# Kernel optimization log

Measured on AMD Instinct MI355X. Metric: run time of the kernel, lower is better.

## Reference

```python
import jax, jax.numpy as jnp
import numpy as np

EPS = 1e-5


def _lstm_agg(x, nbr_idx, Wih, Whh, bih, bhh):
    # x: [N, D] node feats; nbr_idx: [N, K]; LSTM hidden size == D (DGL lstm aggregator)
    seq = x[nbr_idx]                     # [N, K, D] irregular gather
    N, K, D = seq.shape
    seq_t = jnp.swapaxes(seq, 0, 1)      # [K, N, D] time-major for scan

    def step(carry, xt):
        h, c = carry
        z = xt @ Wih.T + bih + h @ Whh.T + bhh   # [N, 4D]; torch gate order i,f,g,o
        i, f, g, o = jnp.split(z, 4, axis=-1)
        i = jax.nn.sigmoid(i)
        f = jax.nn.sigmoid(f)
        g = jnp.tanh(g)
        o = jax.nn.sigmoid(o)
        c = f * c + i * g
        h = o * jnp.tanh(c)
        return (h, c), None

    zero = jnp.zeros((N, D), seq.dtype)
    (h, _), _ = jax.lax.scan(step, (zero, zero), seq_t)
    return h                             # final hidden state = neighbor aggregate


def _sage_layer(x, nbr_idx, Wih, Whh, bih, bhh, Wself, bself, Wneigh):
    h_neigh = _lstm_agg(x, nbr_idx, Wih, Whh, bih, bhh)
    return x @ Wself.T + bself + h_neigh @ Wneigh.T


def _bn(x, gamma, beta):
    # BatchNorm1d in training mode: batch statistics over the node axis
    mu = jnp.mean(x, axis=0)
    var = jnp.var(x, axis=0)
    return (x - mu) * jax.lax.rsqrt(var + EPS) * gamma + beta


def setup_inputs() -> dict:
    key = jax.random.key(0)
    N, K, D_IN, D_H = 100000, 16, 128, 128
    ks = jax.random.split(key, 20)
    s = 0.05
    inp = {
        "in_feat": jax.random.normal(ks[0], (N, D_IN), jnp.float32),
        "nbr_idx": jax.random.randint(ks[1], (N, K), 0, N, jnp.int32),
        # layer 1 (in_feats=128 -> h_feats=128), LSTM hidden = in_feats
        "Wih1": jax.random.normal(ks[2], (4 * D_IN, D_IN), jnp.float32) * s,
        "Whh1": jax.random.normal(ks[3], (4 * D_IN, D_IN), jnp.float32) * s,
        "bih1": jnp.zeros((4 * D_IN,), jnp.float32),
        "bhh1": jnp.zeros((4 * D_IN,), jnp.float32),
        "Wself1": jax.random.normal(ks[4], (D_H, D_IN), jnp.float32) * s,
        "bself1": jnp.zeros((D_H,), jnp.float32),
        "Wneigh1": jax.random.normal(ks[5], (D_H, D_IN), jnp.float32) * s,
        "gamma1": jnp.ones((D_H,), jnp.float32),
        "beta1": jnp.zeros((D_H,), jnp.float32),
        # layer 2 (h_feats=128 -> h_feats=128)
        "Wih2": jax.random.normal(ks[6], (4 * D_H, D_H), jnp.float32) * s,
        "Whh2": jax.random.normal(ks[7], (4 * D_H, D_H), jnp.float32) * s,
        "bih2": jnp.zeros((4 * D_H,), jnp.float32),
        "bhh2": jnp.zeros((4 * D_H,), jnp.float32),
        "Wself2": jax.random.normal(ks[8], (D_H, D_H), jnp.float32) * s,
        "bself2": jnp.zeros((D_H,), jnp.float32),
        "Wneigh2": jax.random.normal(ks[9], (D_H, D_H), jnp.float32) * s,
        "gamma2": jnp.ones((D_H,), jnp.float32),
        "beta2": jnp.zeros((D_H,), jnp.float32),
    }
    return inp


def reference(in_feat, nbr_idx,
              Wih1, Whh1, bih1, bhh1, Wself1, bself1, Wneigh1, gamma1, beta1,
              Wih2, Whh2, bih2, bhh2, Wself2, bself2, Wneigh2, gamma2, beta2):
    h = _sage_layer(in_feat, nbr_idx, Wih1, Whh1, bih1, bhh1, Wself1, bself1, Wneigh1)
    h = jax.nn.relu(_bn(h, gamma1, beta1))
    h = _sage_layer(h, nbr_idx, Wih2, Whh2, bih2, bhh2, Wself2, bself2, Wneigh2)
    h = _bn(h, gamma2, beta2)
    return h
```

## Files before the change

kernel.cpp:

```cpp
#include <hip/hip_runtime.h>

typedef unsigned short u16;
typedef unsigned int u32;
typedef unsigned long long u64;
typedef __attribute__((ext_vector_type(8))) short short8;
typedef __attribute__((ext_vector_type(4))) float float4_t;

__device__ __forceinline__ float bf2f(u16 v) {
    union { u32 u; float f; } x; x.u = ((u32)v) << 16; return x.f;
}
__device__ __forceinline__ u16 f2bf(float f) {
    union { float f; u32 u; } x; x.f = f;
    u32 r = x.u + 0x7FFFu + ((x.u >> 16) & 1u);
    return (u16)(r >> 16);
}
__device__ __forceinline__ u32 pk2bf(float hi, float lo) {
    union { float f; u32 u; } a, b; a.f = hi; b.f = lo;
    return __builtin_amdgcn_perm(a.u + 0x8000u, b.u + 0x8000u, 0x07060302u);
}
#define LOG2E 1.44269504088896340736f
__device__ __forceinline__ float sigm(float x) {
    return __builtin_amdgcn_rcpf(1.f + __builtin_amdgcn_exp2f(-LOG2E * x));
}
__device__ __forceinline__ float tanh_(float x) {
    float t = __builtin_amdgcn_exp2f(2.f * LOG2E * x);
    return 1.f - 2.f * __builtin_amdgcn_rcpf(1.f + t);
}

__device__ __forceinline__ float4_t mfma16(short8 a, short8 b, float4_t c) {
    return __builtin_amdgcn_mfma_f32_16x16x32_bf16(a, b, c, 0, 0, 0);
}

__device__ __forceinline__ short8 ldfrag(const u16* p) { return *(const short8*)p; }
__device__ __forceinline__ short8 ldfrag(const float* p) {
    float4_t a = *(const float4_t*)p;
    float4_t b = *(const float4_t*)(p + 4);
    short8 r;
#pragma unroll
    for (int j = 0; j < 4; ++j) { r[j] = (short)f2bf(a[j]); r[4 + j] = (short)f2bf(b[j]); }
    return r;
}

template<typename AT>
__global__ __launch_bounds__(256) void gemm_ih(
    const AT* __restrict__ A, const float* __restrict__ W,
    const float* __restrict__ b1, const float* __restrict__ b2,
    u16* __restrict__ C, int M)
{
    const int P = 512;
    const int lane = threadIdx.x & 63;
    const int w    = threadIdx.x >> 6;
    const int l15  = lane & 15;
    const int quad = lane >> 4;
    const int rowbase = blockIdx.x * 64;
    const int colbase = blockIdx.y * 128 + w * 32;

    short8 af[4][4];
#pragma unroll
    for (int mb = 0; mb < 4; ++mb) {
        int row = rowbase + mb * 16 + l15;
        if (row >= M) row = M - 1;
        const AT* ap = A + (size_t)row * 128 + quad * 8;
#pragma unroll
        for (int kb = 0; kb < 4; ++kb) af[mb][kb] = ldfrag(ap + kb * 32);
    }
    short8 bfr[2][4];
#pragma unroll
    for (int nb = 0; nb < 2; ++nb) {
        int col = colbase + nb * 16 + l15;
        const float* wp = W + (size_t)col * 128 + quad * 8;
#pragma unroll
        for (int kb = 0; kb < 4; ++kb) bfr[nb][kb] = ldfrag(wp + kb * 32);
    }
    const float4_t z4 = {0.f, 0.f, 0.f, 0.f};
    float bias[2];
#pragma unroll
    for (int nb = 0; nb < 2; ++nb) {
        int col = colbase + nb * 16 + l15;
        bias[nb] = b1[col] + b2[col];
    }
#pragma unroll
    for (int mb = 0; mb < 4; ++mb)
#pragma unroll
        for (int nb = 0; nb < 2; ++nb) {
            float4_t a = z4;
#pragma unroll
            for (int kb = 0; kb < 4; ++kb) a = mfma16(af[mb][kb], bfr[nb][kb], a);
#pragma unroll
            for (int r = 0; r < 4; ++r) {
                int row = rowbase + mb * 16 + quad * 4 + r;
                int col = colbase + nb * 16 + l15;
                if (row < M) C[(size_t)row * P + col] = f2bf(a[r] + bias[nb]);
            }
        }
}

template<typename T>
__device__ __forceinline__ void accum_gemm(
    const T* __restrict__ A, const float* __restrict__ W,
    float4_t (&acc)[4][2], int M, int rowbase, int colbase, int l15, int quad)
{
    short8 af[4][4];
#pragma unroll
    for (int mb = 0; mb < 4; ++mb) {
        int row = rowbase + mb * 16 + l15;
        if (row >= M) row = M - 1;
        const T* ap = A + (size_t)row * 128 + quad * 8;
#pragma unroll
        for (int kb = 0; kb < 4; ++kb) af[mb][kb] = ldfrag(ap + kb * 32);
    }
    short8 bfr[2][4];
#pragma unroll
    for (int nb = 0; nb < 2; ++nb) {
        int col = colbase + nb * 16 + l15;
        const float* wp = W + (size_t)col * 128 + quad * 8;
#pragma unroll
        for (int kb = 0; kb < 4; ++kb) bfr[nb][kb] = ldfrag(wp + kb * 32);
    }
#pragma unroll
    for (int mb = 0; mb < 4; ++mb)
#pragma unroll
        for (int nb = 0; nb < 2; ++nb)
#pragma unroll
            for (int kb = 0; kb < 4; ++kb)
                acc[mb][nb] = mfma16(af[mb][kb], bfr[nb][kb], acc[mb][nb]);
}

template<typename AT2>
__global__ __launch_bounds__(256) void gemm_out(
    const u16* __restrict__ A1, const float* __restrict__ W1,
    const AT2* __restrict__ A2, const float* __restrict__ W2,
    const float* __restrict__ bias, float* __restrict__ C,
    float* __restrict__ stats, int M)
{
    const int P = 128;
    const int lane = threadIdx.x & 63;
    const int w    = threadIdx.x >> 6;
    const int l15  = lane & 15;
    const int quad = lane >> 4;
    const int rowbase = blockIdx.x * 64;
    const int colbase = w * 32;

    float4_t acc[4][2];
    const float4_t z4 = {0.f, 0.f, 0.f, 0.f};
#pragma unroll
    for (int mb = 0; mb < 4; ++mb)
#pragma unroll
        for (int nb = 0; nb < 2; ++nb) acc[mb][nb] = z4;

    accum_gemm(A1, W1, acc, M, rowbase, colbase, l15, quad);
    accum_gemm(A2, W2, acc, M, rowbase, colbase, l15, quad);

    float s[2] = {0.f, 0.f}, sq[2] = {0.f, 0.f};
#pragma unroll
    for (int nb = 0; nb < 2; ++nb) {
        int col = colbase + nb * 16 + l15;
        float bb = bias[col];
#pragma unroll
        for (int mb = 0; mb < 4; ++mb)
#pragma unroll
            for (int r = 0; r < 4; ++r) {
                int row = rowbase + mb * 16 + quad * 4 + r;
                if (row < M) {
                    float v = acc[mb][nb][r] + bb;
                    C[(size_t)row * P + col] = v;
                    s[nb] += v; sq[nb] += v * v;
                }
            }
    }
#pragma unroll
    for (int nb = 0; nb < 2; ++nb) {
        float t1 = s[nb], t2 = sq[nb];
        t1 += __shfl_xor(t1, 16); t1 += __shfl_xor(t1, 32);
        t2 += __shfl_xor(t2, 16); t2 += __shfl_xor(t2, 32);
        int col = colbase + nb * 16 + l15;
        if (quad == 0) atomicAdd(&stats[col], t1);
        if (quad == 1) atomicAdd(&stats[P + col], t2);
    }
}

__global__ __launch_bounds__(512, 2) void lstm_kernel(
    const u16* __restrict__ Xih,
    const int* __restrict__ nbr,
    const float* __restrict__ Whh,
    u16* __restrict__ Hout,
    int N)
{
    __shared__ u16 hbuf[2][64][136];
    __shared__ int nbrs[16][72];
    const int tid  = threadIdx.x;
    const int lane = tid & 63;
    const int w    = tid >> 6;
    const int l15  = lane & 15;
    const int quad = lane >> 4;
    const int base = blockIdx.x * 64;

    short8 whA[4][4];
#pragma unroll
    for (int g = 0; g < 4; ++g) {
        int row = 128 * g + 16 * w + l15;
        const float* wp = Whh + (size_t)row * 128 + quad * 8;
#pragma unroll
        for (int kb = 0; kb < 4; ++kb) whA[g][kb] = ldfrag(wp + kb * 32);
    }
    short8 I;
    {
        int off = (w & 1) ? 16 : 0;
#pragma unroll
        for (int j = 0; j < 8; ++j) {
            int k = quad * 8 + j;
            I[j] = (short)((k == l15 + off) ? 0x3F80 : 0);
        }
    }
    u32* hz = (u32*)&hbuf[0][0][0];
    for (int i = tid; i < 2 * 64 * 136 / 2; i += 512) hz[i] = 0u;
    for (int i = tid; i < 64 * 16; i += 512) {
        int node = base + (i >> 4);
        if (node >= N) node = N - 1;
        nbrs[i & 15][i >> 4] = nbr[(size_t)node * 16 + (i & 15)];
    }
    __syncthreads();

    const int xcol0 = 32 * (w >> 1);
    short8 xf[4][4];
#pragma unroll
    for (int nb = 0; nb < 4; ++nb) {
        int node = nbrs[0][l15 + 16 * nb];
        const u16* xp = Xih + (size_t)node * 512 + xcol0 + quad * 8;
#pragma unroll
        for (int g = 0; g < 4; ++g) xf[nb][g] = *(const short8*)(xp + 128 * g);
    }

    const float4_t z4 = {0.f, 0.f, 0.f, 0.f};
    float4_t c[4];
#pragma unroll
    for (int nb = 0; nb < 4; ++nb) c[nb] = z4;
    float4_t hlast[4];

    for (int t = 0; t < 16; ++t) {
        const int p = t & 1;
#pragma unroll
        for (int nb = 0; nb < 4; ++nb) {
            const u16* hp = &hbuf[p][l15 + 16 * nb][quad * 8];
            short8 hb[4];
#pragma unroll
            for (int kb = 0; kb < 4; ++kb) hb[kb] = *(const short8*)(hp + kb * 32);
            float4_t z[4];
#pragma unroll
            for (int g = 0; g < 4; ++g) z[g] = mfma16(I, xf[nb][g], z4);
            if (t < 15) {
                int node = nbrs[t + 1][l15 + 16 * nb];
                const u16* xp = Xih + (size_t)node * 512 + xcol0 + quad * 8;
#pragma unroll
                for (int g = 0; g < 4; ++g) xf[nb][g] = *(const short8*)(xp + 128 * g);
            }
#pragma unroll
            for (int g = 0; g < 4; ++g)
#pragma unroll
                for (int kb = 0; kb < 4; ++kb)
                    z[g] = mfma16(whA[g][kb], hb[kb], z[g]);
            float4_t hv;
#pragma unroll
            for (int r = 0; r < 4; ++r) {
                float i_ = sigm(z[0][r]);
                float f_ = sigm(z[1][r]);
                float g_ = tanh_(z[2][r]);
                float o_ = sigm(z[3][r]);
                float cc = f_ * c[nb][r] + i_ * g_;
                c[nb][r] = cc;
                hv[r] = o_ * tanh_(cc);
            }
            hlast[nb] = hv;
            u64 pkd = ((u64)pk2bf(hv[3], hv[2]) << 32) | pk2bf(hv[1], hv[0]);
            *(u64*)&hbuf[1 - p][l15 + 16 * nb][16 * w + quad * 4] = pkd;
        }
        __syncthreads();
    }
#pragma unroll
    for (int nb = 0; nb < 4; ++nb) {
        int row = base + l15 + 16 * nb;
        if (row < N) {
            u64 pkd = ((u64)pk2bf(hlast[nb][3], hlast[nb][2]) << 32)
                      | pk2bf(hlast[nb][1], hlast[nb][0]);
            *(u64*)(Hout + (size_t)row * 128 + 16 * w + quad * 4) = pkd;
        }
    }
}

__global__ void zero_stats(float* s) { s[threadIdx.x] = 0.f; }

__global__ void bn_prep(float* stats, const float* __restrict__ gamma,
                        const float* __restrict__ beta, float invN)
{
    int cidx = threadIdx.x;
    float s = stats[cidx], sq = stats[128 + cidx];
    float mu = s * invN;
    float var = sq * invN - mu * mu;
    float sc = gamma[cidx] * rsqrtf(var + 1e-5f);
    stats[256 + cidx] = sc;
    stats[384 + cidx] = beta[cidx] - mu * sc;
}

template<typename OT>
__global__ __launch_bounds__(256) void bn_apply(
    const float* __restrict__ X, const float* __restrict__ stats,
    OT* __restrict__ Y, int M, int relu)
{
    int gid = blockIdx.x * 256 + threadIdx.x;
    int row = gid >> 4;
    int cs  = (gid & 15) * 8;
    if (row >= M) return;
    float4_t a = *(const float4_t*)(X + (size_t)row * 128 + cs);
    float4_t b = *(const float4_t*)(X + (size_t)row * 128 + cs + 4);
    float v[8];
#pragma unroll
    for (int j = 0; j < 8; ++j) {
        float x = (j < 4) ? a[j] : b[j - 4];
        float t = x * stats[256 + cs + j] + stats[384 + cs + j];
        v[j] = relu ? fmaxf(t, 0.f) : t;
    }
    if constexpr (sizeof(OT) == 2) {
        short8 ov;
#pragma unroll
        for (int j = 0; j < 8; ++j) ov[j] = (short)f2bf(v[j]);
        *(short8*)((u16*)Y + (size_t)row * 128 + cs) = ov;
    } else {
        float4_t o1, o2;
#pragma unroll
        for (int j = 0; j < 4; ++j) { o1[j] = v[j]; o2[j] = v[4 + j]; }
        *(float4_t*)((float*)Y + (size_t)row * 128 + cs) = o1;
        *(float4_t*)((float*)Y + (size_t)row * 128 + cs + 4) = o2;
    }
}

extern "C" void kernel_launch(void* const* d_in, const int* in_sizes, int n_in,
                              void* d_out, int out_size, void* d_ws, size_t ws_size,
                              hipStream_t stream)
{
    const float* in_feat = (const float*)d_in[0];
    const int*   nbr     = (const int*)d_in[1];
    const float* Wih1 = (const float*)d_in[2];
    const float* Whh1 = (const float*)d_in[3];
    const float* bih1 = (const float*)d_in[4];
    const float* bhh1 = (const float*)d_in[5];
    const float* Wself1  = (const float*)d_in[6];
    const float* bself1  = (const float*)d_in[7];
    const float* Wneigh1 = (const float*)d_in[8];
    const float* gamma1  = (const float*)d_in[9];
    const float* beta1   = (const float*)d_in[10];
    const float* Wih2 = (const float*)d_in[11];
    const float* Whh2 = (const float*)d_in[12];
    const float* bih2 = (const float*)d_in[13];
    const float* bhh2 = (const float*)d_in[14];
    const float* Wself2  = (const float*)d_in[15];
    const float* bself2  = (const float*)d_in[16];
    const float* Wneigh2 = (const float*)d_in[17];
    const float* gamma2  = (const float*)d_in[18];
    const float* beta2   = (const float*)d_in[19];

    const int N = in_sizes[0] / 128;

    char* ws = (char*)d_ws;
    u16*   Xih   = (u16*)ws;
    float* Pbuf  = (float*)ws;
    u16*   hn    = (u16*)(ws + (size_t)N * 1024);
    float* stats = (float*)(ws + (size_t)N * 1024 + (size_t)N * 256);
    u16*   hcur  = (u16*)d_out;

    const int nblk = (N + 63) / 64;
    const float invN = 1.0f / (float)N;
    const int bnblk = (N * 16 + 255) / 256;

    zero_stats<<<dim3(1), dim3(256), 0, stream>>>(stats);
    gemm_ih<float><<<dim3(nblk, 4), dim3(256), 0, stream>>>(in_feat, Wih1, bih1, bhh1, Xih, N);
    lstm_kernel<<<dim3(nblk), dim3(512), 0, stream>>>(Xih, nbr, Whh1, hn, N);
    gemm_out<float><<<dim3(nblk, 1), dim3(256), 0, stream>>>(hn, Wneigh1, in_feat, Wself1,
                                                             bself1, Pbuf, stats, N);
    bn_prep<<<dim3(1), dim3(128), 0, stream>>>(stats, gamma1, beta1, invN);
    bn_apply<u16><<<dim3(bnblk), dim3(256), 0, stream>>>(Pbuf, stats, hcur, N, 1);

    zero_stats<<<dim3(1), dim3(256), 0, stream>>>(stats);
    gemm_ih<u16><<<dim3(nblk, 4), dim3(256), 0, stream>>>(hcur, Wih2, bih2, bhh2, Xih, N);
    lstm_kernel<<<dim3(nblk), dim3(512), 0, stream>>>(Xih, nbr, Whh2, hn, N);
    gemm_out<u16><<<dim3(nblk, 1), dim3(256), 0, stream>>>(hn, Wneigh2, hcur, Wself2,
                                                           bself2, Pbuf, stats, N);
    bn_prep<<<dim3(1), dim3(128), 0, stream>>>(stats, gamma2, beta2, invN);
    bn_apply<float><<<dim3(bnblk), dim3(256), 0, stream>>>(Pbuf, stats, (float*)d_out, N, 0);
}
```

Before: 1.683 ms.

## Permute Xih columns to match MFMA output layout and add input term directly

The input-projection GEMM now writes its output columns in a permuted order, so each LSTM lane can load its own gate pre-activations with two contiguous 16-byte loads. These values are unpacked from bf16 and added in fp32, which removes the identity-matrix MFMA that was used only to inject the input projection into the accumulator. The change also raises launch bounds to 4 blocks per SM, pads the hidden-state LDS rows to reduce bank conflicts, and moves the barrier to the start of each timestep. Higher occupancy may cause register spills, and correctness now depends on the column permutation matching the lane mapping exactly.

```diff
diff --git a/kernel.cpp b/kernel.cpp
--- a/kernel.cpp
+++ b/kernel.cpp
@@ -5,6 +5,7 @@
 typedef unsigned long long u64;
 typedef __attribute__((ext_vector_type(8))) short short8;
 typedef __attribute__((ext_vector_type(4))) float float4_t;
+typedef __attribute__((ext_vector_type(4))) u32 uint4_t;
 
 __device__ __forceinline__ float bf2f(u16 v) {
     union { u32 u; float f; } x; x.u = ((u32)v) << 16; return x.f;
@@ -39,6 +40,11 @@
 #pragma unroll
     for (int j = 0; j < 4; ++j) { r[j] = (short)f2bf(a[j]); r[4 + j] = (short)f2bf(b[j]); }
     return r;
+}
+
+__device__ __forceinline__ int origcol(int n) {
+    int g = (n >> 2) & 3, w = n >> 6, q = (n >> 4) & 3, r = n & 3;
+    return 128 * g + 16 * w + 4 * q + r;
 }
 
 template<typename AT>
@@ -65,20 +71,16 @@
         for (int kb = 0; kb < 4; ++kb) af[mb][kb] = ldfrag(ap + kb * 32);
     }
     short8 bfr[2][4];
+    float bias[2];
 #pragma unroll
     for (int nb = 0; nb < 2; ++nb) {
-        int col = colbase + nb * 16 + l15;
-        const float* wp = W + (size_t)col * 128 + quad * 8;
+        int ocol = origcol(colbase + nb * 16 + l15);
+        const float* wp = W + (size_t)ocol * 128 + quad * 8;
 #pragma unroll
         for (int kb = 0; kb < 4; ++kb) bfr[nb][kb] = ldfrag(wp + kb * 32);
+        bias[nb] = b1[ocol] + b2[ocol];
     }
     const float4_t z4 = {0.f, 0.f, 0.f, 0.f};
-    float bias[2];
-#pragma unroll
-    for (int nb = 0; nb < 2; ++nb) {
-        int col = colbase + nb * 16 + l15;
-        bias[nb] = b1[col] + b2[col];
-    }
 #pragma unroll
     for (int mb = 0; mb < 4; ++mb)
 #pragma unroll
@@ -179,14 +181,14 @@
     }
 }
 
-__global__ __launch_bounds__(512, 2) void lstm_kernel(
+__global__ __launch_bounds__(512, 4) void lstm_kernel(
     const u16* __restrict__ Xih,
     const int* __restrict__ nbr,
     const float* __restrict__ Whh,
     u16* __restrict__ Hout,
     int N)
 {
-    __shared__ u16 hbuf[2][64][136];
+    __shared__ u16 hbuf[2][64][140];
     __shared__ int nbrs[16][72];
     const int tid  = threadIdx.x;
     const int lane = tid & 63;
@@ -203,17 +205,8 @@
 #pragma unroll
         for (int kb = 0; kb < 4; ++kb) whA[g][kb] = ldfrag(wp + kb * 32);
     }
-    short8 I;
-    {
-        int off = (w & 1) ? 16 : 0;
-#pragma unroll
-        for (int j = 0; j < 8; ++j) {
-            int k = quad * 8 + j;
-            I[j] = (short)((k == l15 + off) ? 0x3F80 : 0);
-        }
-    }
     u32* hz = (u32*)&hbuf[0][0][0];
-    for (int i = tid; i < 2 * 64 * 136 / 2; i += 512) hz[i] = 0u;
+    for (int i = tid; i < 2 * 64 * 70; i += 512) hz[i] = 0u;
     for (int i = tid; i < 64 * 16; i += 512) {
         int node = base + (i >> 4);
         if (node >= N) node = N - 1;
@@ -221,14 +214,12 @@
     }
     __syncthreads();
 
-    const int xcol0 = 32 * (w >> 1);
-    short8 xf[4][4];
+    uint4_t xq[4][2];
 #pragma unroll
     for (int nb = 0; nb < 4; ++nb) {
         int node = nbrs[0][l15 + 16 * nb];
-        const u16* xp = Xih + (size_t)node * 512 + xcol0 + quad * 8;
-#pragma unroll
-        for (int g = 0; g < 4; ++g) xf[nb][g] = *(const short8*)(xp + 128 * g);
+        const uint4_t* xp = (const uint4_t*)(Xih + (size_t)node * 512 + w * 64 + quad * 16);
+        xq[nb][0] = xp[0]; xq[nb][1] = xp[1];
     }
 
     const float4_t z4 = {0.f, 0.f, 0.f, 0.f};
@@ -239,33 +230,45 @@
 
     for (int t = 0; t < 16; ++t) {
         const int p = t & 1;
+        __syncthreads();
 #pragma unroll
         for (int nb = 0; nb < 4; ++nb) {
             const u16* hp = &hbuf[p][l15 + 16 * nb][quad * 8];
-            short8 hb[4];
-#pragma unroll
-            for (int kb = 0; kb < 4; ++kb) hb[kb] = *(const short8*)(hp + kb * 32);
+            short8 hb0 = *(const short8*)(hp);
+            short8 hb1 = *(const short8*)(hp + 32);
+            short8 hb2 = *(const short8*)(hp + 64);
+            short8 hb3 = *(const short8*)(hp + 96);
             float4_t z[4];
 #pragma unroll
-            for (int g = 0; g < 4; ++g) z[g] = mfma16(I, xf[nb][g], z4);
+            for (int g = 0; g < 4; ++g) {
+                float4_t a = mfma16(whA[g][0], hb0, z4);
+                a = mfma16(whA[g][1], hb1, a);
+                a = mfma16(whA[g][2], hb2, a);
+                a = mfma16(whA[g][3], hb3, a);
+                z[g] = a;
+            }
+            float x[4][4];
+#pragma unroll
+            for (int g = 0; g < 4; ++g) {
+                u32 lo = xq[nb][g >> 1][(g & 1) * 2 + 0];
+                u32 hi = xq[nb][g >> 1][(g & 1) * 2 + 1];
+                union { u32 u; float f; } t0, t1, t2, t3;
+                t0.u = lo << 16; t1.u = lo & 0xFFFF0000u;
+                t2.u = hi << 16; t3.u = hi & 0xFFFF0000u;
+                x[g][0] = t0.f; x[g][1] = t1.f; x[g][2] = t2.f; x[g][3] = t3.f;
+            }
             if (t < 15) {
                 int node = nbrs[t + 1][l15 + 16 * nb];
-                const u16* xp = Xih + (size_t)node * 512 + xcol0 + quad * 8;
-#pragma unroll
-                for (int g = 0; g < 4; ++g) xf[nb][g] = *(const short8*)(xp + 128 * g);
-            }
-#pragma unroll
-            for (int g = 0; g < 4; ++g)
-#pragma unroll
-                for (int kb = 0; kb < 4; ++kb)
-                    z[g] = mfma16(whA[g][kb], hb[kb], z[g]);
+                const uint4_t* xp = (const uint4_t*)(Xih + (size_t)node * 512 + w * 64 + quad * 16);
+                xq[nb][0] = xp[0]; xq[nb][1] = xp[1];
+            }
             float4_t hv;
 #pragma unroll
             for (int r = 0; r < 4; ++r) {
-                float i_ = sigm(z[0][r]);
-                float f_ = sigm(z[1][r]);
-                float g_ = tanh_(z[2][r]);
-                float o_ = sigm(z[3][r]);
+                float i_ = sigm(z[0][r] + x[0][r]);
+                float f_ = sigm(z[1][r] + x[1][r]);
+                float g_ = tanh_(z[2][r] + x[2][r]);
+                float o_ = sigm(z[3][r] + x[3][r]);
                 float cc = f_ * c[nb][r] + i_ * g_;
                 c[nb][r] = cc;
                 hv[r] = o_ * tanh_(cc);
@@ -274,7 +277,6 @@
             u64 pkd = ((u64)pk2bf(hv[3], hv[2]) << 32) | pk2bf(hv[1], hv[0]);
             *(u64*)&hbuf[1 - p][l15 + 16 * nb][16 * w + quad * 4] = pkd;
         }
-        __syncthreads();
     }
 #pragma unroll
     for (int nb = 0; nb < 4; ++nb) {
```

Measured after the change: 2.467 ms. 46.6% more time.
